# Performance work log

Measured on AMD Instinct MI355X. Metric: run time of the kernel, lower is better.

The kernel has to match this reference:

```python
import jax, jax.numpy as jnp
import numpy as np

EPS = 1e-5

def _layernorm(x, g, b):
    m = jnp.mean(x, axis=-1, keepdims=True)
    v = jnp.mean((x - m) ** 2, axis=-1, keepdims=True)
    return (x - m) * jax.lax.rsqrt(v + EPS) * g + b

def setup_inputs() -> dict:
    key = jax.random.key(0)
    ks = jax.random.split(key, 6)
    B, N, D, H, F = 4, 4096, 256, 256, 1024
    s = lambda d: 1.0 / np.sqrt(d)
    return {
        "x": jax.random.normal(ks[0], (B, N, D), jnp.float32),
        "ln1_g": jnp.ones((D,), jnp.float32),
        "ln1_b": jnp.zeros((D,), jnp.float32),
        "wq": jax.random.normal(ks[1], (D, H), jnp.float32) * s(D),
        "bq": jnp.zeros((H,), jnp.float32),
        "wk": jax.random.normal(ks[2], (D, H), jnp.float32) * s(D),
        "bk": jnp.zeros((H,), jnp.float32),
        "wv": jax.random.normal(ks[3], (D, D), jnp.float32) * s(D),
        "bv": jnp.zeros((D,), jnp.float32),
        "ln2_g": jnp.ones((D,), jnp.float32),
        "ln2_b": jnp.zeros((D,), jnp.float32),
        "w1": jax.random.normal(ks[4], (D, F), jnp.float32) * s(D),
        "b1": jnp.zeros((F,), jnp.float32),
        "w2": jax.random.normal(ks[5], (F, D), jnp.float32) * s(F),
        "b2": jnp.zeros((D,), jnp.float32),
    }

def reference(x, ln1_g, ln1_b, wq, bq, wk, bk, wv, bv, ln2_g, ln2_b, w1, b1, w2, b2):
    hdim = wq.shape[1]
    x = _layernorm(x, ln1_g, ln1_b)                      # [B,N,D]
    q = x @ wq + bq                                      # [B,N,H]
    k = x @ wk + bk                                      # [B,N,H]
    v = x @ wv + bv                                      # [B,N,D]
    att = jnp.einsum('bnh,bmh->bnm', q, k) / jnp.sqrt(jnp.float32(hdim))
    att = jax.nn.softmax(att, axis=-1)                   # [B,N,N]
    x = jnp.einsum('bnm,bmd->bnd', att, v) + x           # residual around attention
    h = _layernorm(x, ln2_g, ln2_b)
    h = jax.nn.relu(h @ w1 + b1) @ w2 + b2
    return h + x
```

## Files before the change

### kernel.cpp

```cpp
#include <hip/hip_runtime.h>
#include <stdint.h>

typedef unsigned short u16;
typedef __attribute__((ext_vector_type(8))) short short8;
typedef __attribute__((ext_vector_type(4))) float f32x4;
typedef __attribute__((ext_vector_type(16))) float f32x16;

__device__ __forceinline__ u16 f2b(float f){
  union { float f; unsigned u; } x; x.f = f;
  unsigned r = x.u + 0x7FFFu + ((x.u >> 16) & 1u);
  return (u16)(r >> 16);
}

__device__ __forceinline__ unsigned cvtpk_bf16(float lo, float hi){
  unsigned r;
  asm("v_cvt_pk_bf16_f32 %0, %1, %2" : "=v"(r) : "v"(lo), "v"(hi));
  return r;
}

__device__ __forceinline__ void gload_lds16(const void* g, void* l){
  __builtin_amdgcn_global_load_lds(
      (const __attribute__((address_space(1))) unsigned int*)g,
      (__attribute__((address_space(3))) unsigned int*)l, 16, 0, 0);
}

__global__ void __launch_bounds__(256) transpose_all(const float* __restrict__ wq,
                                                     const float* __restrict__ wk,
                                                     const float* __restrict__ wv,
                                                     const float* __restrict__ w1,
                                                     const float* __restrict__ w2,
                                                     u16* __restrict__ wqkvT,
                                                     u16* __restrict__ w1T,
                                                     u16* __restrict__ w2T){
  __shared__ float sm[32][33];
  int id = blockIdx.x;
  const float* in; u16* out; int K, N, kx, ny;
  if (id < 192){
    int j = id >> 6, r = id & 63;
    in = (j==0) ? wq : (j==1) ? wk : wv;
    out = wqkvT + (size_t)j*65536; K = 256; N = 256; kx = r>>3; ny = r&7;
  } else if (id < 448){
    int r = id - 192; in = w1; out = w1T; K = 256; N = 1024; kx = r&7; ny = r>>3;
  } else {
    int r = id - 448; in = w2; out = w2T; K = 1024; N = 256; kx = r>>3; ny = r&7;
  }
  int k0 = kx*32, n0 = ny*32;
  int t = threadIdx.x; int tr = t>>5, tc = t&31;
  #pragma unroll
  for (int p=0;p<4;p++) sm[p*8+tr][tc] = in[(size_t)(k0+p*8+tr)*N + n0+tc];
  __syncthreads();
  #pragma unroll
  for (int p=0;p<4;p++) out[(size_t)(n0+p*8+tr)*K + k0+tc] = f2b(sm[tc][p*8+tr]);
}

__global__ void __launch_bounds__(256) ln_kernel(const float* __restrict__ in,
                                                 const float* __restrict__ g,
                                                 const float* __restrict__ bb,
                                                 float* __restrict__ outF,
                                                 u16* __restrict__ outB){
  int row = blockIdx.x, t = threadIdx.x;
  size_t base = (size_t)row*256;
  float v = in[base + t];
  float s = v;
  #pragma unroll
  for (int m=1;m<64;m<<=1) s += __shfl_xor(s, m);
  __shared__ float red[4];
  int w = t>>6;
  if ((t&63)==0) red[w] = s;
  __syncthreads();
  float mean = (red[0]+red[1]+red[2]+red[3]) * (1.0f/256.0f);
  float d = v - mean;
  float s2 = d*d;
  #pragma unroll
  for (int m=1;m<64;m<<=1) s2 += __shfl_xor(s2, m);
  __syncthreads();
  if ((t&63)==0) red[w] = s2;
  __syncthreads();
  float var = (red[0]+red[1]+red[2]+red[3]) * (1.0f/256.0f);
  float y = d * rsqrtf(var + 1e-5f) * g[t] + bb[t];
  if (outF) outF[base+t] = y;
  outB[base+t] = f2b(y);
}

template<int MODE>
__global__ void __launch_bounds__(256, 2) gemm_bt(const u16* __restrict__ A,
                                                  const u16* __restrict__ BT,
                                                  const float* __restrict__ bias,
                                                  const float* __restrict__ bias2,
                                                  const float* __restrict__ bias3,
                                                  const float* __restrict__ res,
                                                  float* __restrict__ outF,
                                                  u16* __restrict__ outB,
                                                  u16* __restrict__ outB2,
                                                  u16* __restrict__ outB3,
                                                  int M, int N, int K){
  __shared__ u16 As[128*64];
  __shared__ u16 Bs[128*64];
  int tid = threadIdx.x;
  int m0 = blockIdx.x*128, n0 = blockIdx.y*128;
  int wave = tid>>6, lane = tid&63, lr = lane&15, lg = lane>>4;
  int wm = (wave>>1)*64, wn = (wave&1)*64;

  f32x4 acc[4][4];
  #pragma unroll
  for (int i=0;i<4;i++)
    #pragma unroll
    for (int j=0;j<4;j++) acc[i][j] = (f32x4){0.f,0.f,0.f,0.f};

  int nk = K >> 6;
  for (int kt=0; kt<nk; ++kt){
    __syncthreads();
    #pragma unroll
    for (int i=0;i<4;i++){
      int de = i*256 + tid; int row = de>>3; int ch = de&7; int sc = ch ^ (row&7);
      gload_lds16(A + (size_t)(m0+row)*K + kt*64 + sc*8, (char*)As + de*16);
    }
    #pragma unroll
    for (int i=0;i<4;i++){
      int de = i*256 + tid; int row = de>>3; int ch = de&7; int sc = ch ^ (row&7);
      gload_lds16(BT + (size_t)(n0+row)*K + kt*64 + sc*8, (char*)Bs + de*16);
    }
    asm volatile("s_waitcnt vmcnt(0)" ::: "memory");
    __syncthreads();
    #pragma unroll
    for (int kk=0;kk<2;kk++){
      short8 af[4], bf[4];
      #pragma unroll
      for (int mi=0;mi<4;mi++){
        int row = wm + mi*16 + lr;
        int c = (kk*4 + lg) ^ (row&7);
        af[mi] = *(const short8*)&As[row*64 + c*8];
      }
      #pragma unroll
      for (int ni=0;ni<4;ni++){
        int row = wn + ni*16 + lr;
        int c = (kk*4 + lg) ^ (row&7);
        bf[ni] = *(const short8*)&Bs[row*64 + c*8];
      }
      #pragma unroll
      for (int mi=0;mi<4;mi++)
        #pragma unroll
        for (int ni=0;ni<4;ni++)
          acc[mi][ni] = __builtin_amdgcn_mfma_f32_16x16x32_bf16(af[mi], bf[ni], acc[mi][ni], 0,0,0);
    }
  }
  #pragma unroll
  for (int mi=0;mi<4;mi++)
    #pragma unroll
    for (int ni=0;ni<4;ni++)
      #pragma unroll
      for (int r=0;r<4;r++){
        int row = m0 + wm + mi*16 + lg*4 + r;
        int col = n0 + wn + ni*16 + lr;
        if (MODE==3){
          int seg = n0 >> 8;
          int c2 = col & 255;
          float bb = (seg==0) ? bias[c2] : (seg==1) ? bias2[c2] : bias3[c2];
          float vout = acc[mi][ni][r] + bb;
          if (seg==0)      outB [(size_t)row*256 + c2] = f2b(vout);
          else if (seg==1) outB2[(size_t)row*256 + c2] = f2b(vout);
          else {
            size_t gaddr = ((size_t)(row>>12)<<20)
                         + ((((size_t)((row&4095)>>3)<<8) + (size_t)c2)<<3) + (row&7);
            outB3[gaddr] = f2b(vout);
          }
        } else {
          float vout = acc[mi][ni][r] + bias[col];
          if (MODE==1) vout = fmaxf(vout, 0.f);
          if (MODE==2) outF[(size_t)row*N + col] = vout + res[(size_t)row*N + col];
          else         outB[(size_t)row*N + col] = f2b(vout);
        }
      }
}

__device__ __forceinline__ void stage_tiles(const u16* __restrict__ Kb,
                                            const u16* __restrict__ Vt,
                                            int b, int kv0,
                                            char* Kdst, char* Vdst, int tid){
  #pragma unroll
  for (int i=0;i<4;i++){
    int de = i*256 + tid; int kv = de>>5; int c = de&31; int sc = c ^ (kv&7);
    gload_lds16(Kb + (((size_t)(b*4096 + kv0 + kv))<<8) + sc*8, Kdst + (size_t)de*16);
  }
  #pragma unroll
  for (int i=0;i<4;i++){
    int de = i*256 + tid; int kvc = de>>8; int d = de&255;
    gload_lds16(Vt + ((((size_t)b*512 + (kv0>>3) + kvc)<<8) + (size_t)d)*8,
                Vdst + (size_t)de*16);
  }
}

__global__ void __launch_bounds__(256, 2) flash_attn32(const u16* __restrict__ Qb,
                                                       const u16* __restrict__ Kb,
                                                       const u16* __restrict__ Vt,
                                                       u16* __restrict__ Opart,
                                                       float* __restrict__ MLpart){
  __shared__ __align__(16) char smem[74752];
  const int NC = 4096;
  int tid = threadIdx.x, wave = tid>>6, lane = tid&63;
  int lq = lane & 31, hi = lane >> 5;
  int b = blockIdx.y, s = blockIdx.z;
  int qb0 = blockIdx.x*128 + wave*32;
  int kvbeg = s*1024;
  const int NT = 32;
  u16* PsW = (u16*)(smem + 65536) + wave*32*36;

  short8 qf[16];
  {
    const u16* qbase = Qb + (((size_t)b*NC + qb0 + lq)<<8) + hi*8;
    #pragma unroll
    for (int ks=0; ks<16; ks++) qf[ks] = *(const short8*)(qbase + ks*16);
  }

  f32x16 o[8];
  #pragma unroll
  for (int i=0;i<8;i++)
    o[i] = (f32x16){0.f,0.f,0.f,0.f,0.f,0.f,0.f,0.f,0.f,0.f,0.f,0.f,0.f,0.f,0.f,0.f};
  float mrun = -__builtin_inff(), ell = 0.f;

  stage_tiles(Kb, Vt, b, kvbeg, smem, smem + 16384, tid);
  asm volatile("s_waitcnt vmcnt(0)" ::: "memory");
  __syncthreads();

  for (int t=0; t<NT; t++){
    char* Kc = smem + ((t&1) ? 32768 : 0);
    char* Vc = Kc + 16384;
    char* Kn = smem + ((t&1) ? 0 : 32768);
    char* Vn = Kn + 16384;
    int kv0 = kvbeg + t*32;
    if (t+1 < NT) stage_tiles(Kb, Vt, b, kv0+32, Kn, Vn, tid);

    f32x16 sacc  = (f32x16){0.f,0.f,0.f,0.f,0.f,0.f,0.f,0.f,0.f,0.f,0.f,0.f,0.f,0.f,0.f,0.f};
    f32x16 sacc2 = (f32x16){0.f,0.f,0.f,0.f,0.f,0.f,0.f,0.f,0.f,0.f,0.f,0.f,0.f,0.f,0.f,0.f};
    __builtin_amdgcn_s_setprio(1);
    #pragma unroll
    for (int ks=0; ks<8; ks++){
      int c0 = ks*2 + hi;
      int c1 = (ks+8)*2 + hi;
      short8 kf0 = *(const short8*)(Kc + lq*512 + ((c0 ^ (lq&7))<<4));
      short8 kf1 = *(const short8*)(Kc + lq*512 + ((c1 ^ (lq&7))<<4));
      sacc  = __builtin_amdgcn_mfma_f32_32x32x16_bf16(kf0, qf[ks],   sacc,  0,0,0);
      sacc2 = __builtin_amdgcn_mfma_f32_32x32x16_bf16(kf1, qf[ks+8], sacc2, 0,0,0);
    }
    __builtin_amdgcn_s_setprio(0);
    #pragma unroll
    for (int r=0;r<16;r++) sacc[r] += sacc2[r];

    float tmax = sacc[0];
    #pragma unroll
    for (int r=1;r<16;r++) tmax = fmaxf(tmax, sacc[r]);
    tmax *= 0.0625f;
    tmax = fmaxf(tmax, __shfl_xor(tmax, 32));
    if (!__all(tmax <= mrun + 8.f)){
      float mn = fmaxf(mrun, tmax);
      float sc = __expf(mrun - mn);
      mrun = mn; ell *= sc;
      #pragma unroll
      for (int r=0;r<16;r++){
        float scr = __shfl(sc, (r&3)+8*(r>>2)+4*hi);
        #pragma unroll
        for (int dt=0; dt<8; dt++) o[dt][r] *= scr;
      }
    }

    float rs = 0.f;
    #pragma unroll
    for (int h=0; h<2; h++){
      float p[8];
      #pragma unroll
      for (int r=0;r<8;r++){ p[r] = __expf(sacc[h*8+r]*0.0625f - mrun); rs += p[r]; }
      uint2 w0, w1;
      w0.x = cvtpk_bf16(p[0], p[1]);  w0.y = cvtpk_bf16(p[2], p[3]);
      w1.x = cvtpk_bf16(p[4], p[5]);  w1.y = cvtpk_bf16(p[6], p[7]);
      *(uint2*)(PsW + lq*36 + h*16 + hi*4)     = w0;
      *(uint2*)(PsW + lq*36 + h*16 + 8 + hi*4) = w1;
    }
    rs += __shfl_xor(rs, 32);
    ell += rs;
    asm volatile("s_waitcnt lgkmcnt(0)" ::: "memory");
    __builtin_amdgcn_sched_barrier(0);
    union { uint2 u2[2]; short8 s8; } pc0, pc1;
    pc0.u2[0] = *(const uint2*)(PsW + lq*36 + hi*8);
    pc0.u2[1] = *(const uint2*)(PsW + lq*36 + hi*8 + 4);
    pc1.u2[0] = *(const uint2*)(PsW + lq*36 + 16 + hi*8);
    pc1.u2[1] = *(const uint2*)(PsW + lq*36 + 16 + hi*8 + 4);
    short8 pa0 = pc0.s8, pa1 = pc1.s8;

    __builtin_amdgcn_s_setprio(1);
    #pragma unroll
    for (int dt=0; dt<8; dt++){
      short8 vf0 = *(const short8*)(Vc + (((hi  )*256 + dt*32 + lq)<<4));
      short8 vf1 = *(const short8*)(Vc + (((2+hi)*256 + dt*32 + lq)<<4));
      o[dt] = __builtin_amdgcn_mfma_f32_32x32x16_bf16(pa0, vf0, o[dt], 0,0,0);
      o[dt] = __builtin_amdgcn_mfma_f32_32x32x16_bf16(pa1, vf1, o[dt], 0,0,0);
    }
    __builtin_amdgcn_s_setprio(0);

    asm volatile("s_waitcnt vmcnt(0)" ::: "memory");
    __syncthreads();
  }

  size_t rowb = (size_t)s*16384 + (size_t)b*NC + qb0;
  #pragma unroll
  for (int dt=0; dt<8; dt++)
    #pragma unroll
    for (int r=0;r<16;r++){
      int q = (r&3) + 8*(r>>2) + 4*hi;
      Opart[(rowb + q)*256 + dt*32 + lq] = f2b(o[dt][r]);
    }
  if (lane < 32){
    MLpart[(rowb + lane)*2]     = mrun;
    MLpart[(rowb + lane)*2 + 1] = ell;
  }
}

__global__ void __launch_bounds__(256) merge4_ln(const u16* __restrict__ Opart,
                                                 const float* __restrict__ MLpart,
                                                 const float* __restrict__ xln,
                                                 const float* __restrict__ g2,
                                                 const float* __restrict__ be2,
                                                 float* __restrict__ x2,
                                                 u16* __restrict__ h2){
  int row = blockIdx.x; int t = threadIdx.x;
  const size_t RS = 16384ull*256;
  float m[4], l[4];
  #pragma unroll
  for (int s=0;s<4;s++){
    m[s] = MLpart[((size_t)s*16384 + row)*2];
    l[s] = MLpart[((size_t)s*16384 + row)*2 + 1];
  }
  float M = fmaxf(fmaxf(m[0],m[1]), fmaxf(m[2],m[3]));
  float e[4]; float den = 0.f;
  #pragma unroll
  for (int s=0;s<4;s++){ e[s] = __expf(m[s]-M); den += l[s]*e[s]; }
  float inv = 1.0f/den;
  size_t idx = (size_t)row*256 + t;
  float v = 0.f;
  #pragma unroll
  for (int s=0;s<4;s++){
    unsigned u = Opart[(size_t)s*RS + idx];
    v += __uint_as_float(u << 16) * e[s];
  }
  v = v*inv + xln[idx];
  x2[idx] = v;
  float s1 = v;
  #pragma unroll
  for (int mk=1;mk<64;mk<<=1) s1 += __shfl_xor(s1, mk);
  __shared__ float red[4];
  int w = t>>6;
  if ((t&63)==0) red[w] = s1;
  __syncthreads();
  float mean = (red[0]+red[1]+red[2]+red[3]) * (1.0f/256.0f);
  float d = v - mean;
  float s2 = d*d;
  #pragma unroll
  for (int mk=1;mk<64;mk<<=1) s2 += __shfl_xor(s2, mk);
  __syncthreads();
  if ((t&63)==0) red[w] = s2;
  __syncthreads();
  float var = (red[0]+red[1]+red[2]+red[3]) * (1.0f/256.0f);
  h2[idx] = f2b(d * rsqrtf(var + 1e-5f) * g2[t] + be2[t]);
}

extern "C" void kernel_launch(void* const* d_in, const int* in_sizes, int n_in,
                              void* d_out, int out_size, void* d_ws, size_t ws_size,
                              hipStream_t stream){
  const float* x   = (const float*)d_in[0];
  const float* g1  = (const float*)d_in[1];
  const float* be1 = (const float*)d_in[2];
  const float* wq  = (const float*)d_in[3];
  const float* bq  = (const float*)d_in[4];
  const float* wk  = (const float*)d_in[5];
  const float* bk  = (const float*)d_in[6];
  const float* wv  = (const float*)d_in[7];
  const float* bv  = (const float*)d_in[8];
  const float* g2  = (const float*)d_in[9];
  const float* be2 = (const float*)d_in[10];
  const float* w1  = (const float*)d_in[11];
  const float* bm1 = (const float*)d_in[12];
  const float* w2  = (const float*)d_in[13];
  const float* bm2 = (const float*)d_in[14];
  float* out = (float*)d_out;

  const size_t RS = 16384ull*256;
  char* p = (char*)d_ws;
  float* xln = (float*)p;  p += RS*4;
  u16*  Op   = (u16*)p;    p += 4*RS*2;
  float* ML  = (float*)p;  p += 4*16384ull*2*4;
  u16* xb  = (u16*)p; p += RS*2;
  u16* qb  = (u16*)p; p += RS*2;
  u16* kb  = (u16*)p; p += RS*2;
  u16* vT  = (u16*)p; p += RS*2;
  u16* wqkvT = (u16*)p; p += 3*65536ull*2;
  u16* w1T = (u16*)p; p += 262144ull*2;
  u16* w2T = (u16*)p; p += 262144ull*2;
  float* x2 = xln;
  u16*   h1 = Op;
  u16*   h2 = qb;

  transpose_all<<<704, 256, 0, stream>>>(wq, wk, wv, w1, w2, wqkvT, w1T, w2T);

  ln_kernel<<<16384,256,0,stream>>>(x, g1, be1, xln, xb);

  gemm_bt<3><<<dim3(128,6),256,0,stream>>>(xb, wqkvT, bq, bk, bv, nullptr, nullptr,
                                           qb, kb, vT, 16384,768,256);

  flash_attn32<<<dim3(32,4,4),256,0,stream>>>(qb, kb, vT, Op, ML);
  merge4_ln<<<16384,256,0,stream>>>(Op, ML, xln, g2, be2, x2, h2);

  gemm_bt<1><<<dim3(128,8),256,0,stream>>>(h2, w1T, bm1, nullptr, nullptr, nullptr, nullptr,
                                           h1, nullptr, nullptr, 16384,1024,256);
  gemm_bt<2><<<dim3(128,2),256,0,stream>>>(h1, w2T, bm2, nullptr, nullptr, x2, out,
                                           nullptr, nullptr, nullptr, 16384,256,1024);
}
```

Baseline: 181.3 us.

## Software-pipeline QK^T one tile ahead of softmax and PV in flash attention

```diff
diff --git a/kernel.cpp b/kernel.cpp
--- a/kernel.cpp
+++ b/kernel.cpp
@@ -173,15 +173,16 @@
       }
 }
 
-__device__ __forceinline__ void stage_tiles(const u16* __restrict__ Kb,
-                                            const u16* __restrict__ Vt,
-                                            int b, int kv0,
-                                            char* Kdst, char* Vdst, int tid){
+__device__ __forceinline__ void stage_K(const u16* __restrict__ Kb,
+                                        int b, int kv0, char* Kdst, int tid){
   #pragma unroll
   for (int i=0;i<4;i++){
     int de = i*256 + tid; int kv = de>>5; int c = de&31; int sc = c ^ (kv&7);
     gload_lds16(Kb + (((size_t)(b*4096 + kv0 + kv))<<8) + sc*8, Kdst + (size_t)de*16);
   }
+}
+__device__ __forceinline__ void stage_V(const u16* __restrict__ Vt,
+                                        int b, int kv0, char* Vdst, int tid){
   #pragma unroll
   for (int i=0;i<4;i++){
     int de = i*256 + tid; int kvc = de>>8; int d = de&255;
@@ -202,7 +203,10 @@
   int b = blockIdx.y, s = blockIdx.z;
   int qb0 = blockIdx.x*128 + wave*32;
   int kvbeg = s*1024;
-  const int NT = 32;
+  char* Kb0 = smem;
+  char* Kb1 = smem + 16384;
+  char* Vb0 = smem + 32768;
+  char* Vb1 = smem + 49152;
   u16* PsW = (u16*)(smem + 65536) + wave*32*36;
 
   short8 qf[16];
@@ -218,34 +222,20 @@
     o[i] = (f32x16){0.f,0.f,0.f,0.f,0.f,0.f,0.f,0.f,0.f,0.f,0.f,0.f,0.f,0.f,0.f,0.f};
   float mrun = -__builtin_inff(), ell = 0.f;
 
-  stage_tiles(Kb, Vt, b, kvbeg, smem, smem + 16384, tid);
-  asm volatile("s_waitcnt vmcnt(0)" ::: "memory");
-  __syncthreads();
-
-  for (int t=0; t<NT; t++){
-    char* Kc = smem + ((t&1) ? 32768 : 0);
-    char* Vc = Kc + 16384;
-    char* Kn = smem + ((t&1) ? 0 : 32768);
-    char* Vn = Kn + 16384;
-    int kv0 = kvbeg + t*32;
-    if (t+1 < NT) stage_tiles(Kb, Vt, b, kv0+32, Kn, Vn, tid);
-
-    f32x16 sacc  = (f32x16){0.f,0.f,0.f,0.f,0.f,0.f,0.f,0.f,0.f,0.f,0.f,0.f,0.f,0.f,0.f,0.f};
-    f32x16 sacc2 = (f32x16){0.f,0.f,0.f,0.f,0.f,0.f,0.f,0.f,0.f,0.f,0.f,0.f,0.f,0.f,0.f,0.f};
+  auto QKT = [&](const char* Kc) -> f32x16 {
+    f32x16 sa = (f32x16){0.f,0.f,0.f,0.f,0.f,0.f,0.f,0.f,0.f,0.f,0.f,0.f,0.f,0.f,0.f,0.f};
     __builtin_amdgcn_s_setprio(1);
     #pragma unroll
-    for (int ks=0; ks<8; ks++){
-      int c0 = ks*2 + hi;
-      int c1 = (ks+8)*2 + hi;
-      short8 kf0 = *(const short8*)(Kc + lq*512 + ((c0 ^ (lq&7))<<4));
-      short8 kf1 = *(const short8*)(Kc + lq*512 + ((c1 ^ (lq&7))<<4));
-      sacc  = __builtin_amdgcn_mfma_f32_32x32x16_bf16(kf0, qf[ks],   sacc,  0,0,0);
-      sacc2 = __builtin_amdgcn_mfma_f32_32x32x16_bf16(kf1, qf[ks+8], sacc2, 0,0,0);
+    for (int ks=0; ks<16; ks++){
+      int c = ks*2 + hi;
+      short8 kf = *(const short8*)(Kc + lq*512 + ((c ^ (lq&7))<<4));
+      sa = __builtin_amdgcn_mfma_f32_32x32x16_bf16(kf, qf[ks], sa, 0,0,0);
     }
     __builtin_amdgcn_s_setprio(0);
-    #pragma unroll
-    for (int r=0;r<16;r++) sacc[r] += sacc2[r];
-
+    return sa;
+  };
+
+  auto SOFTMAX_PV = [&](f32x16& sacc, const char* Vc){
     float tmax = sacc[0];
     #pragma unroll
     for (int r=1;r<16;r++) tmax = fmaxf(tmax, sacc[r]);
@@ -262,7 +252,6 @@
         for (int dt=0; dt<8; dt++) o[dt][r] *= scr;
       }
     }
-
     float rs = 0.f;
     #pragma unroll
     for (int h=0; h<2; h++){
@@ -285,7 +274,6 @@
     pc1.u2[0] = *(const uint2*)(PsW + lq*36 + 16 + hi*8);
     pc1.u2[1] = *(const uint2*)(PsW + lq*36 + 16 + hi*8 + 4);
     short8 pa0 = pc0.s8, pa1 = pc1.s8;
-
     __builtin_amdgcn_s_setprio(1);
     #pragma unroll
     for (int dt=0; dt<8; dt++){
@@ -295,7 +283,28 @@
       o[dt] = __builtin_amdgcn_mfma_f32_32x32x16_bf16(pa1, vf1, o[dt], 0,0,0);
     }
     __builtin_amdgcn_s_setprio(0);
-
+  };
+
+  stage_K(Kb, b, kvbeg,      Kb0, tid);
+  stage_V(Vt, b, kvbeg,      Vb0, tid);
+  stage_K(Kb, b, kvbeg + 32, Kb1, tid);
+  asm volatile("s_waitcnt vmcnt(0)" ::: "memory");
+  __syncthreads();
+
+  f32x16 saccA = QKT(Kb0);
+
+  for (int tt=0; tt<16; tt++){
+    int t = tt*2;
+    f32x16 saccB = QKT(Kb1);
+    if (t+2 < 32) stage_K(Kb, b, kvbeg + (t+2)*32, Kb0, tid);
+    stage_V(Vt, b, kvbeg + (t+1)*32, Vb1, tid);
+    SOFTMAX_PV(saccA, Vb0);
+    asm volatile("s_waitcnt vmcnt(0)" ::: "memory");
+    __syncthreads();
+    if (t+2 < 32) saccA = QKT(Kb0);
+    if (t+3 < 32) stage_K(Kb, b, kvbeg + (t+3)*32, Kb1, tid);
+    if (t+2 < 32) stage_V(Vt, b, kvbeg + (t+2)*32, Vb0, tid);
+    SOFTMAX_PV(saccB, Vb1);
     asm volatile("s_waitcnt vmcnt(0)" ::: "memory");
     __syncthreads();
   }
```

Result: slower. 219.2 us (+20.9%).
